# Kernel tuning notes

Hardware: AMD Instinct MI355X
Metric: run time of the kernel (lower is better)

The kernel has to match this reference:

```python
import jax, jax.numpy as jnp
import numpy as np

B, S, D = 2, 2048, 1024
H, DH = 16, 64
C = 64          # chunk_size (sliding window)
WF = 4          # widening factor
FMIN = jnp.finfo(jnp.float32).min


def _ln(x, scale, offset, eps=1e-5):
    mu = jnp.mean(x, axis=-1, keepdims=True)
    var = jnp.var(x, axis=-1, keepdims=True)
    return (x - mu) * jax.lax.rsqrt(var + eps) * scale + offset


def setup_inputs() -> dict:
    key = jax.random.key(0)
    ks = jax.random.split(key, 12)
    std = 0.02
    inp = {
        'x': jax.random.normal(ks[0], (B, S, D), dtype=jnp.float32),
        'causal_mask': jnp.tril(jnp.ones((S, S), dtype=bool))[None, None],  # (1,1,S,S)
        'pos': jax.random.normal(ks[1], (C, D), dtype=jnp.float32),          # pos_0..pos_{C-1}
        'rpe': std * jax.random.normal(ks[2], (H, C), dtype=jnp.float32),
        'Wq': std * jax.random.normal(ks[3], (D, H * DH), dtype=jnp.float32),
        'Wk': std * jax.random.normal(ks[4], (D, H * DH), dtype=jnp.float32),
        'Wv': std * jax.random.normal(ks[5], (D, H * DH), dtype=jnp.float32),
        'Wo': std * jax.random.normal(ks[6], (H * DH, D), dtype=jnp.float32),
        'ln1_scale': jnp.ones((D,), jnp.float32),
        'ln1_offset': jnp.zeros((D,), jnp.float32),
        'W1': std * jax.random.normal(ks[7], (D, WF * D), dtype=jnp.float32),
        'b1': jnp.zeros((WF * D,), jnp.float32),
        'W2': std * jax.random.normal(ks[8], (WF * D, D), dtype=jnp.float32),
        'b2': jnp.zeros((D,), jnp.float32),
        'ln2_scale': jnp.ones((D,), jnp.float32),
        'ln2_offset': jnp.zeros((D,), jnp.float32),
    }
    return inp


def _sliding_window_mask(rpe, seq_len):
    # mask[h,t,T] = rpe[h, t-T] if 0 <= t-T < C (lower diagonals), else -inf
    d = jnp.arange(seq_len)[:, None] - jnp.arange(seq_len)[None, :]  # (S,S)
    valid = (d >= 0) & (d < C)
    dc = jnp.clip(d, 0, C - 1)
    val = jnp.where(valid[None], rpe[:, dc], 0.0)  # (H,S,S)
    return jnp.where(val != 0, val, FMIN)


def reference(x, causal_mask, pos, rpe, Wq, Wk, Wv, Wo, ln1_scale, ln1_offset,
              W1, b1, W2, b2, ln2_scale, ln2_offset):
    seq_len = x.shape[1]
    # front/rear positional vectors: pos_i added at positions i, i+C, i+2C, ...
    h = x + pos[jnp.arange(seq_len) % C]  # (B,S,D)

    q = (h @ Wq).reshape(B, seq_len, H, DH)
    k = (h @ Wk).reshape(B, seq_len, H, DH)
    v = (h @ Wv).reshape(B, seq_len, H, DH)

    attn = jnp.einsum('bthd,bThd->bhtT', q, k) * (1.0 / jnp.sqrt(DH))
    attn = attn + _sliding_window_mask(rpe, seq_len)[None]  # learned diag bias
    attn = jnp.where(causal_mask, attn, FMIN)
    attn = jax.nn.softmax(attn, axis=-1)

    out = jnp.einsum('bhtT,bThd->bthd', attn, v).reshape(B, seq_len, H * DH)
    out = out @ Wo

    # dropout_prob = 0 -> identity
    attention = _ln(h + out, ln1_scale, ln1_offset)
    ff = jax.nn.relu(attention @ W1 + b1) @ W2 + b2
    return _ln(ff + attention, ln2_scale, ln2_offset)
```

## Files before the change

### kernel.cpp

```cpp
#include <hip/hip_runtime.h>
#include <hip/hip_bf16.h>

#define DEVI static __device__ __forceinline__

typedef __attribute__((ext_vector_type(4))) float f32x4;
typedef __attribute__((ext_vector_type(8))) short bf16x8;
typedef __attribute__((ext_vector_type(4))) short s16x4;

constexpr int TB  = 2;
constexpr int TS  = 2048;
constexpr int TD  = 1024;
constexpr int TH  = 16;
constexpr int TDH = 64;
constexpr int TC  = 64;
constexpr int TFF = 4096;
constexpr int TM  = TB * TS;

DEVI float bf2f(short s) {
  return __builtin_bit_cast(float, (unsigned)((unsigned short)s) << 16);
}
DEVI short f2bf(float f) {
  return __builtin_bit_cast(short, __float2bfloat16(f));
}

#define GLD16(gp, lp)                                              \
  __builtin_amdgcn_global_load_lds(                                \
      (const __attribute__((address_space(1))) void*)(gp),         \
      (__attribute__((address_space(3))) void*)(lp), 16, 0, 0)

#define WAITVM(N) asm volatile("s_waitcnt vmcnt(" #N ")" ::: "memory")

__global__ __launch_bounds__(256) void k_trans_all(
    const float* __restrict__ Wq, const float* __restrict__ Wk,
    const float* __restrict__ Wv, const float* __restrict__ Wo,
    const float* __restrict__ W1, const float* __restrict__ W2,
    __hip_bfloat16* __restrict__ WqkvT, __hip_bfloat16* __restrict__ WoT,
    __hip_bfloat16* __restrict__ W1T, __hip_bfloat16* __restrict__ W2T,
    const float* __restrict__ x, const float* __restrict__ pos,
    __hip_bfloat16* __restrict__ hb) {
  int bid = blockIdx.x;
  if (bid >= 12288) {
    int i = (bid - 12288) * 256 + threadIdx.x;
    int e = i * 4;
    int d = e & (TD - 1);
    int t = (e / TD) & (TS - 1);
    f32x4 xv = *(const f32x4*)(x + e);
    f32x4 pv = *(const f32x4*)(pos + (size_t)(t & (TC - 1)) * TD + d);
    s16x4 hb4;
    for (int j = 0; j < 4; j++) hb4[j] = f2bf(xv[j] + pv[j]);
    *(s16x4*)((short*)hb + e) = hb4;
    return;
  }
  __shared__ float tile[32][33];
  const float* src; __hip_bfloat16* dst;
  int K, N, n0, k0;
  if (bid < 4096) {
    int m = bid >> 10, t = bid & 1023;
    src = (m == 0) ? Wq : (m == 1) ? Wk : (m == 2) ? Wv : Wo;
    dst = (m == 3) ? WoT : WqkvT + (size_t)m * TD * TD;
    K = TD; N = TD; n0 = (t & 31) * 32; k0 = (t >> 5) * 32;
  } else if (bid < 8192) {
    int t = bid - 4096;
    src = W1; dst = W1T; K = TD; N = TFF;
    n0 = (t & 127) * 32; k0 = (t >> 7) * 32;
  } else {
    int t = bid - 8192;
    src = W2; dst = W2T; K = TFF; N = TD;
    n0 = (t & 31) * 32; k0 = (t >> 5) * 32;
  }
  int tx = threadIdx.x & 31, ty = threadIdx.x >> 5;
  for (int i = 0; i < 32; i += 8)
    tile[ty + i][tx] = src[(size_t)(k0 + ty + i) * N + n0 + tx];
  __syncthreads();
  for (int i = 0; i < 32; i += 8)
    dst[(size_t)(n0 + ty + i) * K + k0 + tx] = __float2bfloat16(tile[tx][ty + i]);
}

template <int BN, int EPI>
__global__ __launch_bounds__(512, 2) void k_gemm8(
    const __hip_bfloat16* __restrict__ A, const __hip_bfloat16* __restrict__ BT,
    void* __restrict__ Cout, const float* __restrict__ bias,
    int M, int N, int K, int lda, int ldb) {
  constexpr int BM = 256, BK = 32;
  constexpr int FN = BN / 64;
  __shared__ __align__(16) short As[4][BM * BK];
  __shared__ __align__(16) short Bs[4][BN * BK];
  int tid = threadIdx.x, lane = tid & 63, wave = tid >> 6;
  int wm = wave >> 2, wn = wave & 3;
  int fr = lane & 15, fg = lane >> 4;

  int bx, by, bz;
  {
    int gx = gridDim.x, gy = gridDim.y;
    int nb = gx * gy * gridDim.z;
    int phys = blockIdx.x + gx * (blockIdx.y + gy * blockIdx.z);
    int chunk = nb >> 3;
    int logical = (phys & 7) * chunk + (phys >> 3);
    int perz = gx * gy;
    bz = logical / perz;
    int l2 = logical - bz * perz;
    int g = l2 / (8 * gy);
    int r = l2 - g * 8 * gy;
    by = r >> 3;
    bx = g * 8 + (r & 7);
  }
  int m0 = bx * BM, n0 = by * BN;
  size_t koff = (size_t)bz * K;
  const short* Ab = (const short*)A + koff;
  const short* Bb = (const short*)BT + koff;

  int r0 = tid >> 2, s0 = (tid & 3) ^ ((r0 >> 1) & 3);
  int r1 = 128 + r0, s1 = (tid & 3) ^ ((r1 >> 1) & 3);
  const short* pA0 = Ab + (size_t)(m0 + r0) * lda + s0 * 8;
  const short* pA1 = Ab + (size_t)(m0 + r1) * lda + s1 * 8;
  const short* pB0 = Bb + (size_t)(n0 + r0) * ldb + s0 * 8;
  const short* pB1 = (BN == 256) ? Bb + (size_t)(n0 + r1) * ldb + s1 * 8 : pB0;
  int dst0 = (wave * 64) * 16;
  int dst1 = (512 + wave * 64) * 16;

  auto stageA = [&](int d, int T) {
    GLD16(pA0 + T * BK, (char*)&As[d][0] + dst0);
    GLD16(pA1 + T * BK, (char*)&As[d][0] + dst1);
  };
  auto stageB = [&](int d, int T) {
    GLD16(pB0 + T * BK, (char*)&Bs[d][0] + dst0);
    if constexpr (BN == 256) GLD16(pB1 + T * BK, (char*)&Bs[d][0] + dst1);
  };

  f32x4 acc[8][FN];
#pragma unroll
  for (int m = 0; m < 8; m++)
#pragma unroll
    for (int n = 0; n < FN; n++) acc[m][n] = f32x4{0.f, 0.f, 0.f, 0.f};

  const int nt = K / BK;
  stageA(0, 0); stageB(0, 0);
  stageA(1, 1); stageB(1, 1);
  stageA(2, 2); stageB(2, 2);
  if (BN == 256) { WAITVM(8); } else { WAITVM(6); }
  __builtin_amdgcn_s_barrier();

  for (int t = 0; t < nt; t++) {
    int d = t & 3, pf = (t + 3) & 3;
    bool dopf = (t + 3) < nt;
    const char* Al = (const char*)&As[d][0];
    const char* Bl = (const char*)&Bs[d][0];
    if constexpr (BN == 256) {
      bf16x8 a[4], b[4];
#pragma unroll
      for (int mt = 0; mt < 4; mt++) {
        int row = wm * 128 + mt * 16 + fr;
        a[mt] = *(const bf16x8*)(Al + row * 64 + ((fg ^ ((row >> 1) & 3)) << 4));
      }
#pragma unroll
      for (int n = 0; n < 4; n++) {
        int row = wn * 64 + n * 16 + fr;
        b[n] = *(const bf16x8*)(Bl + row * 64 + ((fg ^ ((row >> 1) & 3)) << 4));
      }
      if (dopf) stageA(pf, t + 3);
      __builtin_amdgcn_s_barrier();
      __builtin_amdgcn_s_setprio(1);
#pragma unroll
      for (int mt = 0; mt < 4; mt++)
#pragma unroll
        for (int n = 0; n < 4; n++)
          acc[mt][n] = __builtin_amdgcn_mfma_f32_16x16x32_bf16(a[mt], b[n],
                                                               acc[mt][n], 0, 0, 0);
      __builtin_amdgcn_s_setprio(0);
      __builtin_amdgcn_s_barrier();
#pragma unroll
      for (int mt = 0; mt < 4; mt++) {
        int row = wm * 128 + 64 + mt * 16 + fr;
        a[mt] = *(const bf16x8*)(Al + row * 64 + ((fg ^ ((row >> 1) & 3)) << 4));
      }
      if (dopf) stageB(pf, t + 3);
      if (t < nt - 3) { WAITVM(8); }
      else if (t == nt - 3) { WAITVM(4); }
      else if (t == nt - 2) { WAITVM(0); }
      __builtin_amdgcn_s_barrier();
      __builtin_amdgcn_s_setprio(1);
#pragma unroll
      for (int mt = 0; mt < 4; mt++)
#pragma unroll
        for (int n = 0; n < 4; n++)
          acc[4 + mt][n] = __builtin_amdgcn_mfma_f32_16x16x32_bf16(a[mt], b[n],
                                                                   acc[4 + mt][n], 0, 0, 0);
      __builtin_amdgcn_s_setprio(0);
      __builtin_amdgcn_s_barrier();
    } else {
      bf16x8 a[8], b[2];
#pragma unroll
      for (int mt = 0; mt < 8; mt++) {
        int row = wm * 128 + mt * 16 + fr;
        a[mt] = *(const bf16x8*)(Al + row * 64 + ((fg ^ ((row >> 1) & 3)) << 4));
      }
#pragma unroll
      for (int n = 0; n < 2; n++) {
        int row = wn * 32 + n * 16 + fr;
        b[n] = *(const bf16x8*)(Bl + row * 64 + ((fg ^ ((row >> 1) & 3)) << 4));
      }
      if (dopf) { stageA(pf, t + 3); stageB(pf, t + 3); }
      if (t < nt - 3) { WAITVM(6); }
      else if (t == nt - 3) { WAITVM(3); }
      else if (t == nt - 2) { WAITVM(0); }
      __builtin_amdgcn_s_barrier();
      __builtin_amdgcn_s_setprio(1);
#pragma unroll
      for (int mt = 0; mt < 8; mt++)
#pragma unroll
        for (int n = 0; n < 2; n++)
          acc[mt][n] = __builtin_amdgcn_mfma_f32_16x16x32_bf16(a[mt], b[n],
                                                               acc[mt][n], 0, 0, 0);
      __builtin_amdgcn_s_setprio(0);
      __builtin_amdgcn_s_barrier();
    }
  }

#pragma unroll
  for (int mt = 0; mt < 8; mt++)
#pragma unroll
    for (int n = 0; n < FN; n++) {
      int col = n0 + wn * (BN / 4) + n * 16 + fr;
      float bv = (EPI == 1) ? bias[col] : 0.f;
#pragma unroll
      for (int j = 0; j < 4; j++) {
        int row = m0 + wm * 128 + mt * 16 + fg * 4 + j;
        float v = acc[mt][n][j];
        if (EPI == 1) { v += bv; v = fmaxf(v, 0.f); }
        if (EPI == 2)
          ((__hip_bfloat16*)Cout)[(size_t)bz * M * N + (size_t)row * N + col] =
              __float2bfloat16(v);
        else
          ((__hip_bfloat16*)Cout)[(size_t)row * N + col] = __float2bfloat16(v);
      }
    }
}

__global__ __launch_bounds__(256) void k_vtrans(
    const __hip_bfloat16* __restrict__ qkv, __hip_bfloat16* __restrict__ vT) {
  __shared__ short tile[64][68];
  int bh = blockIdx.x;
  int tb = blockIdx.y;
  int b = bh >> 4, h = bh & 15;
  int tid = threadIdx.x;
#pragma unroll
  for (int i = 0; i < 2; i++) {
    int c = i * 256 + tid;
    int trow = c >> 3, seg = c & 7;
    bf16x8 v = *(const bf16x8*)((const short*)qkv +
        (size_t)(b * TS + tb * 64 + trow) * 3072 + 2048 + h * TDH + seg * 8);
    s16x4 lo = {v[0], v[1], v[2], v[3]}, hi = {v[4], v[5], v[6], v[7]};
    *(s16x4*)&tile[trow][seg * 8] = lo;
    *(s16x4*)&tile[trow][seg * 8 + 4] = hi;
  }
  __syncthreads();
#pragma unroll
  for (int i2 = 0; i2 < 2; i2++) {
    int c = i2 * 256 + tid;
    int d = c >> 3, ts = c & 7;
    bf16x8 o;
#pragma unroll
    for (int j = 0; j < 8; j++) o[j] = tile[ts * 8 + j][d];
    *(bf16x8*)((short*)vT + (size_t)bh * TDH * TS + (size_t)d * TS +
               tb * 64 + ts * 8) = o;
  }
}

__global__ __launch_bounds__(256) void k_attn(
    const __hip_bfloat16* __restrict__ qkv, const __hip_bfloat16* __restrict__ vT,
    const float* __restrict__ rpe, __hip_bfloat16* __restrict__ out) {
  __shared__ __align__(16) short K_lds[128 * 64];
  __shared__ __align__(16) short VT_lds[64 * 128];
  __shared__ __align__(16) short P_lds[4][16 * 136];
  __shared__ float rpe_lds[TC];
  int tid = threadIdx.x, lane = tid & 63, wave = tid >> 6;
  int fr = lane & 15, g = lane >> 4;
  int blk = blockIdx.x;
  int qt = blk & 31, bh = blk >> 5;
  int h = bh & 15, b = bh >> 4;
  int t0 = qt * 64;
  const short* qg = (const short*)qkv;

  if (tid < TC) rpe_lds[tid] = rpe[h * TC + tid];

#pragma unroll
  for (int i = 0; i < 4; i++) {
    int cb = i * 256 + wave * 64;
    int c = cb + lane;
    int row = c >> 3, slot = c & 7;
    int seg = slot ^ (row & 7);
    int kr = t0 - 64 + row; if (kr < 0) kr = 0;
    GLD16(qg + ((size_t)(b * TS + kr) * 3072 + 1024 + h * TDH + seg * 8),
          (char*)K_lds + cb * 16);
  }
  const short* vg = (const short*)vT + (size_t)bh * TDH * TS;
#pragma unroll
  for (int i = 0; i < 4; i++) {
    int cb = i * 256 + wave * 64;
    int c = cb + lane;
    int row = c >> 4, slot = c & 15;
    int seg = slot ^ (row & 15);
    int tc = t0 - 64 + seg * 8; if (tc < 0) tc = 0;
    GLD16(vg + (size_t)row * TS + tc, (char*)VT_lds + cb * 16);
  }

  int qrow = t0 + wave * 16 + fr;
  const short* qptr = qg + ((size_t)(b * TS + qrow) * 3072 + h * TDH + g * 8);
  bf16x8 qf0 = *(const bf16x8*)qptr;
  bf16x8 qf1 = *(const bf16x8*)(qptr + 32);

  __syncthreads();

  f32x4 S[8] = {};
#pragma unroll
  for (int kk = 0; kk < 2; kk++) {
    bf16x8 a = kk ? qf1 : qf0;
#pragma unroll
    for (int nt = 0; nt < 8; nt++) {
      int row = nt * 16 + fr;
      int slot = (kk * 4 + g) ^ (row & 7);
      bf16x8 bfrag = *(const bf16x8*)((const char*)K_lds + row * 128 + slot * 16);
      S[nt] = __builtin_amdgcn_mfma_f32_16x16x32_bf16(a, bfrag, S[nt], 0, 0, 0);
    }
  }

  int wq = wave * 16;
#pragma unroll
  for (int r = 0; r < 4; r++) {
    int ql = g * 4 + r;
    float sc[8];
    float m = -3.4028235e38f;
#pragma unroll
    for (int nt = 0; nt < 8; nt++) {
      int jj = nt * 16 + fr;
      int d = wq + ql + 64 - jj;
      bool valid = (d >= 0) && (d < TC) && (t0 - 64 + jj >= 0);
      float v = valid ? (S[nt][r] * 0.125f + rpe_lds[d & (TC - 1)])
                      : -3.4028235e38f;
      sc[nt] = v;
      m = fmaxf(m, v);
    }
#pragma unroll
    for (int o = 1; o < 16; o <<= 1) m = fmaxf(m, __shfl_xor(m, o));
    float p[8], sum = 0.f;
#pragma unroll
    for (int nt = 0; nt < 8; nt++) { p[nt] = __expf(sc[nt] - m); sum += p[nt]; }
#pragma unroll
    for (int o = 1; o < 16; o <<= 1) sum += __shfl_xor(sum, o);
    float rs = 1.0f / sum;
#pragma unroll
    for (int nt = 0; nt < 8; nt++)
      P_lds[wave][ql * 136 + nt * 16 + fr] = f2bf(p[nt] * rs);
  }

  f32x4 O[4] = {};
#pragma unroll
  for (int kk = 0; kk < 4; kk++) {
    bf16x8 pa = *(const bf16x8*)((const char*)&P_lds[wave][0] +
                                 fr * 272 + kk * 64 + g * 16);
#pragma unroll
    for (int dt = 0; dt < 4; dt++) {
      int row = dt * 16 + fr;
      int slot = (kk * 4 + g) ^ (row & 15);
      bf16x8 vb = *(const bf16x8*)((const char*)VT_lds + row * 256 + slot * 16);
      O[dt] = __builtin_amdgcn_mfma_f32_16x16x32_bf16(pa, vb, O[dt], 0, 0, 0);
    }
  }

  size_t ob = ((size_t)(b * TS + t0 + wq + g * 4)) * TD + h * TDH;
#pragma unroll
  for (int dt = 0; dt < 4; dt++)
#pragma unroll
    for (int r = 0; r < 4; r++)
      ((short*)out)[ob + (size_t)r * TD + dt * 16 + fr] = f2bf(O[dt][r]);
}

DEVI float block_sum(float v, float* red) {
  for (int o = 32; o; o >>= 1) v += __shfl_xor(v, o);
  int wave = threadIdx.x >> 6;
  if ((threadIdx.x & 63) == 0) red[wave] = v;
  __syncthreads();
  float r = red[0] + red[1] + red[2] + red[3];
  __syncthreads();
  return r;
}

__global__ __launch_bounds__(256) void k_ln1(
    const __hip_bfloat16* __restrict__ hB, const __hip_bfloat16* __restrict__ P0,
    const __hip_bfloat16* __restrict__ P1, const float* __restrict__ scale,
    const float* __restrict__ offset, float* __restrict__ outf,
    __hip_bfloat16* __restrict__ outb) {
  __shared__ float red[4];
  int row = blockIdx.x, tid = threadIdx.x;
  size_t base = (size_t)row * TD + tid * 4;
  s16x4 hv = *(const s16x4*)((const short*)hB + base);
  s16x4 a0 = *(const s16x4*)((const short*)P0 + base);
  s16x4 a1 = *(const s16x4*)((const short*)P1 + base);
  f32x4 xv;
  for (int j = 0; j < 4; j++) xv[j] = bf2f(hv[j]) + bf2f(a0[j]) + bf2f(a1[j]);
  float s = xv[0] + xv[1] + xv[2] + xv[3];
  s = block_sum(s, red);
  float mu = s * (1.f / TD);
  float s2 = 0.f;
  for (int j = 0; j < 4; j++) { float dlt = xv[j] - mu; s2 += dlt * dlt; }
  s2 = block_sum(s2, red);
  float rs = rsqrtf(s2 * (1.f / TD) + 1e-5f);
  f32x4 sc = *(const f32x4*)(scale + tid * 4);
  f32x4 of = *(const f32x4*)(offset + tid * 4);
  f32x4 y;
  for (int j = 0; j < 4; j++) y[j] = (xv[j] - mu) * rs * sc[j] + of[j];
  *(f32x4*)(outf + base) = y;
  s16x4 pb;
  for (int j = 0; j < 4; j++) pb[j] = f2bf(y[j]);
  *(s16x4*)((short*)outb + base) = pb;
}

__global__ __launch_bounds__(256) void k_ln2(
    const __hip_bfloat16* __restrict__ P0, const __hip_bfloat16* __restrict__ P1,
    const float* __restrict__ R, const float* __restrict__ bias,
    const float* __restrict__ scale, const float* __restrict__ offset,
    float* __restrict__ outf) {
  __shared__ float red[4];
  int row = blockIdx.x, tid = threadIdx.x;
  size_t base = (size_t)row * TD + tid * 4;
  s16x4 a0 = *(const s16x4*)((const short*)P0 + base);
  s16x4 a1 = *(const s16x4*)((const short*)P1 + base);
  f32x4 rv = *(const f32x4*)(R + base);
  f32x4 bi = *(const f32x4*)(bias + tid * 4);
  f32x4 xv;
  for (int j = 0; j < 4; j++) xv[j] = bf2f(a0[j]) + bf2f(a1[j]) + rv[j] + bi[j];
  float s = xv[0] + xv[1] + xv[2] + xv[3];
  s = block_sum(s, red);
  float mu = s * (1.f / TD);
  float s2 = 0.f;
  for (int j = 0; j < 4; j++) { float dlt = xv[j] - mu; s2 += dlt * dlt; }
  s2 = block_sum(s2, red);
  float rs = rsqrtf(s2 * (1.f / TD) + 1e-5f);
  f32x4 sc = *(const f32x4*)(scale + tid * 4);
  f32x4 of = *(const f32x4*)(offset + tid * 4);
  f32x4 y;
  for (int j = 0; j < 4; j++) y[j] = (xv[j] - mu) * rs * sc[j] + of[j];
  *(f32x4*)(outf + base) = y;
}

extern "C" void kernel_launch(void* const* d_in, const int* in_sizes, int n_in,
                              void* d_out, int out_size, void* d_ws, size_t ws_size,
                              hipStream_t stream) {
  const float* x    = (const float*)d_in[0];
  const float* pos  = (const float*)d_in[2];
  const float* rpe  = (const float*)d_in[3];
  const float* Wq   = (const float*)d_in[4];
  const float* Wk   = (const float*)d_in[5];
  const float* Wv   = (const float*)d_in[6];
  const float* Wo   = (const float*)d_in[7];
  const float* ln1s = (const float*)d_in[8];
  const float* ln1o = (const float*)d_in[9];
  const float* W1   = (const float*)d_in[10];
  const float* b1   = (const float*)d_in[11];
  const float* W2   = (const float*)d_in[12];
  const float* b2   = (const float*)d_in[13];
  const float* ln2s = (const float*)d_in[14];
  const float* ln2o = (const float*)d_in[15];

  char* ws = (char*)d_ws;
  const size_t MB = 1ull << 20;
  __hip_bfloat16* WqkvT = (__hip_bfloat16*)(ws + 0 * MB);
  __hip_bfloat16* WoT   = (__hip_bfloat16*)(ws + 6 * MB);
  __hip_bfloat16* W1T   = (__hip_bfloat16*)(ws + 8 * MB);
  __hip_bfloat16* W2T   = (__hip_bfloat16*)(ws + 16 * MB);
  __hip_bfloat16* hB    = (__hip_bfloat16*)(ws + 24 * MB);
  __hip_bfloat16* qkv   = (__hip_bfloat16*)(ws + 32 * MB);
  __hip_bfloat16* aoB   = (__hip_bfloat16*)(ws + 56 * MB);
  __hip_bfloat16* oB2   = (__hip_bfloat16*)(ws + 64 * MB);
  float*          atF   = (float*)(ws + 96 * MB);
  __hip_bfloat16* atB   = (__hip_bfloat16*)(ws + 24 * MB);
  __hip_bfloat16* ff1   = (__hip_bfloat16*)(ws + 32 * MB);
  __hip_bfloat16* ff2   = (__hip_bfloat16*)(ws + 64 * MB);
  __hip_bfloat16* vTb   = (__hip_bfloat16*)(ws + 112 * MB);

  dim3 blk(256), blk5(512);

  k_trans_all<<<16384, blk, 0, stream>>>(Wq, Wk, Wv, Wo, W1, W2,
                                         WqkvT, WoT, W1T, W2T, x, pos, hB);

  k_gemm8<256, 0><<<dim3(TM / 256, 3072 / 256, 1), blk5, 0, stream>>>(
      hB, WqkvT, qkv, nullptr, TM, 3072, TD, TD, TD);

  k_vtrans<<<dim3(TB * TH, TS / 64), blk, 0, stream>>>(qkv, vTb);
  k_attn<<<TB * TH * (TS / 64), blk, 0, stream>>>(qkv, vTb, rpe, aoB);

  k_gemm8<128, 2><<<dim3(TM / 256, TD / 128, 2), blk5, 0, stream>>>(
      aoB, WoT, oB2, nullptr, TM, TD, TD / 2, TD, TD);

  k_ln1<<<TM, blk, 0, stream>>>(hB, oB2, oB2 + (size_t)TM * TD, ln1s, ln1o,
                                atF, atB);

  k_gemm8<256, 1><<<dim3(TM / 256, TFF / 256, 1), blk5, 0, stream>>>(
      atB, W1T, ff1, b1, TM, TFF, TD, TD, TD);

  k_gemm8<128, 2><<<dim3(TM / 256, TD / 128, 2), blk5, 0, stream>>>(
      ff1, W2T, ff2, nullptr, TM, TD, TFF / 2, TFF, TFF);

  k_ln2<<<TM, blk, 0, stream>>>(ff2, ff2 + (size_t)TM * TD, atF, b2, ln2s, ln2o,
                                (float*)d_out);
}
```

Baseline: 197.9 us.

## Add BK=64 double-buffered 256x256 GEMM and use 4-way split-K for FFN2

```diff
diff --git a/kernel.cpp b/kernel.cpp
--- a/kernel.cpp
+++ b/kernel.cpp
@@ -29,6 +29,21 @@
       (__attribute__((address_space(3))) void*)(lp), 16, 0, 0)
 
 #define WAITVM(N) asm volatile("s_waitcnt vmcnt(" #N ")" ::: "memory")
+
+DEVI void xcd_remap(int& bx, int& by, int& bz) {
+  int gx = gridDim.x, gy = gridDim.y;
+  int nb = gx * gy * gridDim.z;
+  int phys = blockIdx.x + gx * (blockIdx.y + gy * blockIdx.z);
+  int chunk = nb >> 3;
+  int logical = (phys & 7) * chunk + (phys >> 3);
+  int perz = gx * gy;
+  bz = logical / perz;
+  int l2 = logical - bz * perz;
+  int g = l2 / (8 * gy);
+  int r = l2 - g * 8 * gy;
+  by = r >> 3;
+  bx = g * 8 + (r & 7);
+}
 
 __global__ __launch_bounds__(256) void k_trans_all(
     const float* __restrict__ Wq, const float* __restrict__ Wk,
@@ -76,6 +91,164 @@
     dst[(size_t)(n0 + ty + i) * K + k0 + tx] = __float2bfloat16(tile[tx][ty + i]);
 }
 
+template <int EPI>
+__global__ __launch_bounds__(512, 2) void k_g64(
+    const __hip_bfloat16* __restrict__ A, const __hip_bfloat16* __restrict__ BT,
+    void* __restrict__ Cout, const float* __restrict__ bias,
+    int M, int N, int K, int lda, int ldb) {
+  constexpr int BM = 256, BK = 64;
+  __shared__ __align__(16) short As[2][2][128 * 64];
+  __shared__ __align__(16) short Bs[2][2][128 * 64];
+  int tid = threadIdx.x, lane = tid & 63, wave = tid >> 6;
+  int wm = wave >> 2, wn = wave & 3;
+  int fr = lane & 15, fg = lane >> 4;
+  int bx, by, bz;
+  xcd_remap(bx, by, bz);
+  int m0 = bx * BM, n0 = by * 256;
+  size_t koff = (size_t)bz * K;
+  const short* Ab = (const short*)A + koff;
+  const short* Bb = (const short*)BT + koff;
+
+  int srow0 = tid >> 3, soct0 = (tid & 7) ^ (srow0 & 7);
+  int srow1 = 64 + srow0, soct1 = (tid & 7) ^ (srow1 & 7);
+  int dst0 = (wave * 64) * 16, dst1 = (512 + wave * 64) * 16;
+
+  auto stA = [&](int db, int hf, int T) {
+    GLD16(Ab + (size_t)(m0 + hf * 128 + srow0) * lda + T * BK + soct0 * 8,
+          (char*)&As[db][hf][0] + dst0);
+    GLD16(Ab + (size_t)(m0 + hf * 128 + srow1) * lda + T * BK + soct1 * 8,
+          (char*)&As[db][hf][0] + dst1);
+  };
+  auto stB = [&](int db, int hf, int T) {
+    GLD16(Bb + (size_t)(n0 + hf * 128 + srow0) * ldb + T * BK + soct0 * 8,
+          (char*)&Bs[db][hf][0] + dst0);
+    GLD16(Bb + (size_t)(n0 + hf * 128 + srow1) * ldb + T * BK + soct1 * 8,
+          (char*)&Bs[db][hf][0] + dst1);
+  };
+
+  f32x4 acc[8][4];
+#pragma unroll
+  for (int m = 0; m < 8; m++)
+#pragma unroll
+    for (int n = 0; n < 4; n++) acc[m][n] = f32x4{0.f, 0.f, 0.f, 0.f};
+
+  const int nt = K / BK;
+  stA(0, 0, 0); stA(0, 1, 0); stB(0, 0, 0); stB(0, 1, 0);
+  stA(1, 0, 1); stA(1, 1, 1); stB(1, 0, 1); stB(1, 1, 1);
+  WAITVM(8);
+  __builtin_amdgcn_s_barrier();
+
+  int bbase = (wn & 1) * 64;
+  for (int t = 0; t < nt; t++) {
+    int db = t & 1;
+    const char* Ah = (const char*)&As[db][wm][0];
+    const char* Bh = (const char*)&Bs[db][wn >> 1][0];
+    bf16x8 alo[2][4], ahi[2][4], blo[2][2], bhi[2][2];
+#pragma unroll
+    for (int ks = 0; ks < 2; ks++)
+#pragma unroll
+      for (int mt = 0; mt < 4; mt++) {
+        int row = mt * 16 + fr;
+        alo[ks][mt] = *(const bf16x8*)(Ah + row * 128 +
+                                       (((ks * 4 + fg) ^ (row & 7)) << 4));
+      }
+#pragma unroll
+    for (int ks = 0; ks < 2; ks++)
+#pragma unroll
+      for (int n = 0; n < 2; n++) {
+        int row = bbase + n * 16 + fr;
+        blo[ks][n] = *(const bf16x8*)(Bh + row * 128 +
+                                      (((ks * 4 + fg) ^ (row & 7)) << 4));
+      }
+    __builtin_amdgcn_s_barrier();
+    __builtin_amdgcn_s_setprio(1);
+#pragma unroll
+    for (int ks = 0; ks < 2; ks++)
+#pragma unroll
+      for (int mt = 0; mt < 4; mt++)
+#pragma unroll
+        for (int n = 0; n < 2; n++)
+          acc[mt][n] = __builtin_amdgcn_mfma_f32_16x16x32_bf16(
+              alo[ks][mt], blo[ks][n], acc[mt][n], 0, 0, 0);
+    __builtin_amdgcn_s_setprio(0);
+    __builtin_amdgcn_s_barrier();
+#pragma unroll
+    for (int ks = 0; ks < 2; ks++)
+#pragma unroll
+      for (int n = 0; n < 2; n++) {
+        int row = bbase + (n + 2) * 16 + fr;
+        bhi[ks][n] = *(const bf16x8*)(Bh + row * 128 +
+                                      (((ks * 4 + fg) ^ (row & 7)) << 4));
+      }
+    __builtin_amdgcn_s_barrier();
+    __builtin_amdgcn_s_setprio(1);
+#pragma unroll
+    for (int ks = 0; ks < 2; ks++)
+#pragma unroll
+      for (int mt = 0; mt < 4; mt++)
+#pragma unroll
+        for (int n = 0; n < 2; n++)
+          acc[mt][n + 2] = __builtin_amdgcn_mfma_f32_16x16x32_bf16(
+              alo[ks][mt], bhi[ks][n], acc[mt][n + 2], 0, 0, 0);
+    __builtin_amdgcn_s_setprio(0);
+    __builtin_amdgcn_s_barrier();
+#pragma unroll
+    for (int ks = 0; ks < 2; ks++)
+#pragma unroll
+      for (int mt = 0; mt < 4; mt++) {
+        int row = (mt + 4) * 16 + fr;
+        ahi[ks][mt] = *(const bf16x8*)(Ah + row * 128 +
+                                       (((ks * 4 + fg) ^ (row & 7)) << 4));
+      }
+    if (t + 2 < nt) { stB(db, 0, t + 2); stB(db, 1, t + 2); }
+    __builtin_amdgcn_s_barrier();
+    __builtin_amdgcn_s_setprio(1);
+#pragma unroll
+    for (int ks = 0; ks < 2; ks++)
+#pragma unroll
+      for (int mt = 0; mt < 4; mt++)
+#pragma unroll
+        for (int n = 0; n < 2; n++)
+          acc[mt + 4][n] = __builtin_amdgcn_mfma_f32_16x16x32_bf16(
+              ahi[ks][mt], blo[ks][n], acc[mt + 4][n], 0, 0, 0);
+    __builtin_amdgcn_s_setprio(0);
+    __builtin_amdgcn_s_barrier();
+    if (t + 2 < nt) { stA(db, 0, t + 2); stA(db, 1, t + 2); }
+    __builtin_amdgcn_s_barrier();
+    __builtin_amdgcn_s_setprio(1);
+#pragma unroll
+    for (int ks = 0; ks < 2; ks++)
+#pragma unroll
+      for (int mt = 0; mt < 4; mt++)
+#pragma unroll
+        for (int n = 0; n < 2; n++)
+          acc[mt + 4][n + 2] = __builtin_amdgcn_mfma_f32_16x16x32_bf16(
+              ahi[ks][mt], bhi[ks][n], acc[mt + 4][n + 2], 0, 0, 0);
+    __builtin_amdgcn_s_setprio(0);
+    if (t + 2 < nt) { WAITVM(8); } else { WAITVM(0); }
+    __builtin_amdgcn_s_barrier();
+  }
+
+#pragma unroll
+  for (int mt = 0; mt < 8; mt++)
+#pragma unroll
+    for (int n = 0; n < 4; n++) {
+      int col = n0 + wn * 64 + n * 16 + fr;
+      float bv = (EPI == 1) ? bias[col] : 0.f;
+#pragma unroll
+      for (int j = 0; j < 4; j++) {
+        int row = m0 + wm * 128 + mt * 16 + fg * 4 + j;
+        float v = acc[mt][n][j];
+        if (EPI == 1) { v += bv; v = fmaxf(v, 0.f); }
+        if (EPI == 2)
+          ((__hip_bfloat16*)Cout)[(size_t)bz * M * N + (size_t)row * N + col] =
+              __float2bfloat16(v);
+        else
+          ((__hip_bfloat16*)Cout)[(size_t)row * N + col] = __float2bfloat16(v);
+      }
+    }
+}
+
 template <int BN, int EPI>
 __global__ __launch_bounds__(512, 2) void k_gemm8(
     const __hip_bfloat16* __restrict__ A, const __hip_bfloat16* __restrict__ BT,
@@ -88,22 +261,8 @@
   int tid = threadIdx.x, lane = tid & 63, wave = tid >> 6;
   int wm = wave >> 2, wn = wave & 3;
   int fr = lane & 15, fg = lane >> 4;
-
   int bx, by, bz;
-  {
-    int gx = gridDim.x, gy = gridDim.y;
-    int nb = gx * gy * gridDim.z;
-    int phys = blockIdx.x + gx * (blockIdx.y + gy * blockIdx.z);
-    int chunk = nb >> 3;
-    int logical = (phys & 7) * chunk + (phys >> 3);
-    int perz = gx * gy;
-    bz = logical / perz;
-    int l2 = logical - bz * perz;
-    int g = l2 / (8 * gy);
-    int r = l2 - g * 8 * gy;
-    by = r >> 3;
-    bx = g * 8 + (r & 7);
-  }
+  xcd_remap(bx, by, bz);
   int m0 = bx * BM, n0 = by * BN;
   size_t koff = (size_t)bz * K;
   const short* Ab = (const short*)A + koff;
@@ -145,75 +304,31 @@
     bool dopf = (t + 3) < nt;
     const char* Al = (const char*)&As[d][0];
     const char* Bl = (const char*)&Bs[d][0];
-    if constexpr (BN == 256) {
-      bf16x8 a[4], b[4];
-#pragma unroll
-      for (int mt = 0; mt < 4; mt++) {
-        int row = wm * 128 + mt * 16 + fr;
-        a[mt] = *(const bf16x8*)(Al + row * 64 + ((fg ^ ((row >> 1) & 3)) << 4));
-      }
-#pragma unroll
-      for (int n = 0; n < 4; n++) {
-        int row = wn * 64 + n * 16 + fr;
-        b[n] = *(const bf16x8*)(Bl + row * 64 + ((fg ^ ((row >> 1) & 3)) << 4));
-      }
-      if (dopf) stageA(pf, t + 3);
-      __builtin_amdgcn_s_barrier();
-      __builtin_amdgcn_s_setprio(1);
-#pragma unroll
-      for (int mt = 0; mt < 4; mt++)
-#pragma unroll
-        for (int n = 0; n < 4; n++)
-          acc[mt][n] = __builtin_amdgcn_mfma_f32_16x16x32_bf16(a[mt], b[n],
-                                                               acc[mt][n], 0, 0, 0);
-      __builtin_amdgcn_s_setprio(0);
-      __builtin_amdgcn_s_barrier();
-#pragma unroll
-      for (int mt = 0; mt < 4; mt++) {
-        int row = wm * 128 + 64 + mt * 16 + fr;
-        a[mt] = *(const bf16x8*)(Al + row * 64 + ((fg ^ ((row >> 1) & 3)) << 4));
-      }
-      if (dopf) stageB(pf, t + 3);
-      if (t < nt - 3) { WAITVM(8); }
-      else if (t == nt - 3) { WAITVM(4); }
-      else if (t == nt - 2) { WAITVM(0); }
-      __builtin_amdgcn_s_barrier();
-      __builtin_amdgcn_s_setprio(1);
-#pragma unroll
-      for (int mt = 0; mt < 4; mt++)
-#pragma unroll
-        for (int n = 0; n < 4; n++)
-          acc[4 + mt][n] = __builtin_amdgcn_mfma_f32_16x16x32_bf16(a[mt], b[n],
-                                                                   acc[4 + mt][n], 0, 0, 0);
-      __builtin_amdgcn_s_setprio(0);
-      __builtin_amdgcn_s_barrier();
-    } else {
-      bf16x8 a[8], b[2];
-#pragma unroll
-      for (int mt = 0; mt < 8; mt++) {
-        int row = wm * 128 + mt * 16 + fr;
-        a[mt] = *(const bf16x8*)(Al + row * 64 + ((fg ^ ((row >> 1) & 3)) << 4));
-      }
-#pragma unroll
-      for (int n = 0; n < 2; n++) {
-        int row = wn * 32 + n * 16 + fr;
-        b[n] = *(const bf16x8*)(Bl + row * 64 + ((fg ^ ((row >> 1) & 3)) << 4));
-      }
-      if (dopf) { stageA(pf, t + 3); stageB(pf, t + 3); }
-      if (t < nt - 3) { WAITVM(6); }
-      else if (t == nt - 3) { WAITVM(3); }
-      else if (t == nt - 2) { WAITVM(0); }
-      __builtin_amdgcn_s_barrier();
-      __builtin_amdgcn_s_setprio(1);
-#pragma unroll
-      for (int mt = 0; mt < 8; mt++)
-#pragma unroll
-        for (int n = 0; n < 2; n++)
-          acc[mt][n] = __builtin_amdgcn_mfma_f32_16x16x32_bf16(a[mt], b[n],
-                                                               acc[mt][n], 0, 0, 0);
-      __builtin_amdgcn_s_setprio(0);
-      __builtin_amdgcn_s_barrier();
+    bf16x8 a[8], b[2];
+#pragma unroll
+    for (int mt = 0; mt < 8; mt++) {
+      int row = wm * 128 + mt * 16 + fr;
+      a[mt] = *(const bf16x8*)(Al + row * 64 + ((fg ^ ((row >> 1) & 3)) << 4));
     }
+#pragma unroll
+    for (int n = 0; n < 2; n++) {
+      int row = wn * 32 + n * 16 + fr;
+      b[n] = *(const bf16x8*)(Bl + row * 64 + ((fg ^ ((row >> 1) & 3)) << 4));
+    }
+    if (dopf) { stageA(pf, t + 3); stageB(pf, t + 3); }
+    if (t < nt - 3) { WAITVM(6); }
+    else if (t == nt - 3) { WAITVM(3); }
+    else if (t == nt - 2) { WAITVM(0); }
+    __builtin_amdgcn_s_barrier();
+    __builtin_amdgcn_s_setprio(1);
+#pragma unroll
+    for (int mt = 0; mt < 8; mt++)
+#pragma unroll
+      for (int n = 0; n < 2; n++)
+        acc[mt][n] = __builtin_amdgcn_mfma_f32_16x16x32_bf16(a[mt], b[n],
+                                                             acc[mt][n], 0, 0, 0);
+    __builtin_amdgcn_s_setprio(0);
+    __builtin_amdgcn_s_barrier();
   }
 
 #pragma unroll
@@ -417,6 +532,7 @@
 
 __global__ __launch_bounds__(256) void k_ln2(
     const __hip_bfloat16* __restrict__ P0, const __hip_bfloat16* __restrict__ P1,
+    const __hip_bfloat16* __restrict__ P2, const __hip_bfloat16* __restrict__ P3,
     const float* __restrict__ R, const float* __restrict__ bias,
     const float* __restrict__ scale, const float* __restrict__ offset,
     float* __restrict__ outf) {
@@ -425,10 +541,13 @@
   size_t base = (size_t)row * TD + tid * 4;
   s16x4 a0 = *(const s16x4*)((const short*)P0 + base);
   s16x4 a1 = *(const s16x4*)((const short*)P1 + base);
+  s16x4 a2 = *(const s16x4*)((const short*)P2 + base);
+  s16x4 a3 = *(const s16x4*)((const short*)P3 + base);
   f32x4 rv = *(const f32x4*)(R + base);
   f32x4 bi = *(const f32x4*)(bias + tid * 4);
   f32x4 xv;
-  for (int j = 0; j < 4; j++) xv[j] = bf2f(a0[j]) + bf2f(a1[j]) + rv[j] + bi[j];
+  for (int j = 0; j < 4; j++)
+    xv[j] = bf2f(a0[j]) + bf2f(a1[j]) + bf2f(a2[j]) + bf2f(a3[j]) + rv[j] + bi[j];
   float s = xv[0] + xv[1] + xv[2] + xv[3];
   s = block_sum(s, red);
   float mu = s * (1.f / TD);
@@ -483,7 +602,7 @@
   k_trans_all<<<16384, blk, 0, stream>>>(Wq, Wk, Wv, Wo, W1, W2,
                                          WqkvT, WoT, W1T, W2T, x, pos, hB);
 
-  k_gemm8<256, 0><<<dim3(TM / 256, 3072 / 256, 1), blk5, 0, stream>>>(
+  k_g64<0><<<dim3(TM / 256, 3072 / 256, 1), blk5, 0, stream>>>(
       hB, WqkvT, qkv, nullptr, TM, 3072, TD, TD, TD);
 
   k_vtrans<<<dim3(TB * TH, TS / 64), blk, 0, stream>>>(qkv, vTb);
@@ -495,12 +614,13 @@
   k_ln1<<<TM, blk, 0, stream>>>(hB, oB2, oB2 + (size_t)TM * TD, ln1s, ln1o,
                                 atF, atB);
 
-  k_gemm8<256, 1><<<dim3(TM / 256, TFF / 256, 1), blk5, 0, stream>>>(
+  k_g64<1><<<dim3(TM / 256, TFF / 256, 1), blk5, 0, stream>>>(
       atB, W1T, ff1, b1, TM, TFF, TD, TD, TD);
 
-  k_gemm8<128, 2><<<dim3(TM / 256, TD / 128, 2), blk5, 0, stream>>>(
-      ff1, W2T, ff2, nullptr, TM, TD, TFF / 2, TFF, TFF);
-
-  k_ln2<<<TM, blk, 0, stream>>>(ff2, ff2 + (size_t)TM * TD, atF, b2, ln2s, ln2o,
-                                (float*)d_out);
-}
+  k_g64<2><<<dim3(TM / 256, TD / 256, 4), blk5, 0, stream>>>(
+      ff1, W2T, ff2, nullptr, TM, TD, TFF / 4, TFF, TFF);
+
+  k_ln2<<<TM, blk, 0, stream>>>(ff2, ff2 + (size_t)TM * TD,
+                                ff2 + (size_t)2 * TM * TD, ff2 + (size_t)3 * TM * TD,
+                                atF, b2, ln2s, ln2o, (float*)d_out);
+}
```

After: 189.8 us. 1.04x faster.
